# Optimization experiments

Hardware: AMD Instinct MI355X
Metric: run time of the kernel (lower is better)

## Reference

```python
import jax, jax.numpy as jnp
import numpy as np

D_MODEL = 1024
NUM_HEADS = 16
HEAD_DIM = D_MODEL // NUM_HEADS


def setup_inputs() -> dict:
    key = jax.random.key(0)
    k1, k2, k3 = jax.random.split(key, 3)
    B, T = 4, 2048
    x = jax.random.normal(k1, (B, T, D_MODEL), dtype=jnp.float32)
    # nn.Linear weights: out = x @ W.T; store torch-layout [out_features, in_features]
    w_qkv = jax.random.normal(k2, (3 * D_MODEL, D_MODEL), dtype=jnp.float32) * (D_MODEL ** -0.5)
    w_proj = jax.random.normal(k3, (D_MODEL, D_MODEL), dtype=jnp.float32) * (D_MODEL ** -0.5)
    return {"x": x, "w_qkv": w_qkv, "w_proj": w_proj}


def reference(x, w_qkv, w_proj):
    B, T, C = x.shape
    H, Dh = NUM_HEADS, HEAD_DIM
    qkv = jnp.einsum('btc,fc->btf', x, w_qkv)          # [B,T,3C]
    q, k, v = jnp.split(qkv, 3, axis=2)
    # [B,T,C] -> [B,H,T,Dh]
    q = q.reshape(B, T, H, Dh).transpose(0, 2, 1, 3)
    k = k.reshape(B, T, H, Dh).transpose(0, 2, 1, 3)
    v = v.reshape(B, T, H, Dh).transpose(0, 2, 1, 3)
    scale = Dh ** -0.5
    att = jnp.einsum('bhqd,bhkd->bhqk', q, k) * scale  # [B,H,T,T]
    causal = jnp.tril(jnp.ones((T, T), dtype=bool))
    att = jnp.where(causal, att, -jnp.inf)
    att = jax.nn.softmax(att, axis=-1)
    y = jnp.einsum('bhqk,bhkd->bhqd', att, v)          # [B,H,T,Dh]
    y = y.transpose(0, 2, 1, 3).reshape(B, T, C)
    return jnp.einsum('btc,oc->bto', y, w_proj)
```

## Files before the change

### kernel.cpp

```cpp
#include <hip/hip_runtime.h>
#include <stdint.h>
#include <math.h>

typedef __bf16 bf16;
typedef __bf16 bf16x4 __attribute__((ext_vector_type(4)));
typedef __bf16 bf16x8 __attribute__((ext_vector_type(8)));
typedef float f32x4 __attribute__((ext_vector_type(4)));

#define MFMA16(a, b, c) __builtin_amdgcn_mfma_f32_16x16x32_bf16((a), (b), (c), 0, 0, 0)

typedef __attribute__((address_space(1))) void* as1v;
typedef __attribute__((address_space(3))) void* as3v;

__device__ __forceinline__ void async_ld16(const void* g, void* l) {
  __builtin_amdgcn_global_load_lds((as1v)(uintptr_t)g,
                                   (as3v)(unsigned int)(uintptr_t)l, 16, 0, 0);
}

__global__ __launch_bounds__(256) void cast3_k(const float* __restrict__ x,
                                               const float* __restrict__ wq,
                                               const float* __restrict__ wp,
                                               bf16* __restrict__ xb,
                                               bf16* __restrict__ wqb,
                                               bf16* __restrict__ wpb) {
  const long i = (long)blockIdx.x * 256 + threadIdx.x;
  const float4* src;
  bf16x4* dst;
  long off;
  if (i < 2097152L) {
    src = (const float4*)x;  dst = (bf16x4*)xb;  off = i;
  } else if (i < 2097152L + 786432L) {
    src = (const float4*)wq; dst = (bf16x4*)wqb; off = i - 2097152L;
  } else {
    src = (const float4*)wp; dst = (bf16x4*)wpb; off = i - 2097152L - 786432L;
  }
  float4 v = src[off];
  bf16x4 o;
  o[0] = (bf16)v.x; o[1] = (bf16)v.y; o[2] = (bf16)v.z; o[3] = (bf16)v.w;
  dst[off] = o;
}

__global__ __launch_bounds__(256) void gemm_qkv(const bf16* __restrict__ A,
                                                const bf16* __restrict__ Bm,
                                                bf16* __restrict__ qb,
                                                bf16* __restrict__ kb,
                                                bf16* __restrict__ vth) {
  __shared__ bf16 As[128 * 32];
  __shared__ bf16 Bs[128 * 32];
  const int tid  = threadIdx.x;
  const int lane = tid & 63;
  const int wv   = tid >> 6;
  const int lr   = lane & 15;
  const int quad = lane >> 4;
  const int wm   = (wv >> 1) * 64;
  const int wn   = (wv & 1) * 64;
  const long m0 = (long)blockIdx.y * 128;
  const long n0 = (long)blockIdx.x * 128;

  const f32x4 fzero = {0.f, 0.f, 0.f, 0.f};
  f32x4 acc[4][4];
#pragma unroll
  for (int i = 0; i < 4; ++i)
#pragma unroll
    for (int j = 0; j < 4; ++j) acc[i][j] = fzero;

  const int r0 = wv * 32 + (lane >> 2);
  const int c0 = (lane & 3) * 8;

  for (int k0 = 0; k0 < 1024; k0 += 32) {
    __syncthreads();
    async_ld16(&A[(m0 + r0) * 1024 + k0 + c0],        &As[wv * 1024]);
    async_ld16(&A[(m0 + r0 + 16) * 1024 + k0 + c0],   &As[wv * 1024 + 512]);
    async_ld16(&Bm[(n0 + r0) * 1024 + k0 + c0],       &Bs[wv * 1024]);
    async_ld16(&Bm[(n0 + r0 + 16) * 1024 + k0 + c0],  &Bs[wv * 1024 + 512]);
    __syncthreads();

    bf16x8 af[4], bfr[4];
#pragma unroll
    for (int mi = 0; mi < 4; ++mi)
      af[mi] = *(const bf16x8*)&As[(wm + mi * 16 + lr) * 32 + quad * 8];
#pragma unroll
    for (int ni = 0; ni < 4; ++ni)
      bfr[ni] = *(const bf16x8*)&Bs[(wn + ni * 16 + lr) * 32 + quad * 8];
#pragma unroll
    for (int mi = 0; mi < 4; ++mi)
#pragma unroll
      for (int ni = 0; ni < 4; ++ni)
        acc[mi][ni] = MFMA16(af[mi], bfr[ni], acc[mi][ni]);
  }

  const int bx = blockIdx.x;
  if (bx < 8) {
    const float kS = 0.18033688f;
#pragma unroll
    for (int mi = 0; mi < 4; ++mi) {
      const long row = m0 + wm + mi * 16 + quad * 4;
#pragma unroll
      for (int ni = 0; ni < 4; ++ni) {
        const long col = n0 + wn + ni * 16 + lr;
#pragma unroll
        for (int r = 0; r < 4; ++r) qb[(row + r) * 1024 + col] = (bf16)(acc[mi][ni][r] * kS);
      }
    }
  } else if (bx < 16) {
#pragma unroll
    for (int mi = 0; mi < 4; ++mi) {
      const long row = m0 + wm + mi * 16 + quad * 4;
#pragma unroll
      for (int ni = 0; ni < 4; ++ni) {
        const long col = n0 + wn + ni * 16 + lr - 1024;
#pragma unroll
        for (int r = 0; r < 4; ++r) kb[(row + r) * 1024 + col] = (bf16)(acc[mi][ni][r]);
      }
    }
  } else {
#pragma unroll
    for (int mi = 0; mi < 4; ++mi) {
      const long row = m0 + wm + mi * 16 + quad * 4;
      const long b = row >> 11;
      const long t = row & 2047;
#pragma unroll
      for (int ni = 0; ni < 4; ++ni) {
        const long vcol = n0 + wn + ni * 16 + lr - 2048;
        const long h = vcol >> 6, d = vcol & 63;
        bf16x4 pk;
#pragma unroll
        for (int r = 0; r < 4; ++r) pk[r] = (bf16)(acc[mi][ni][r]);
        *(bf16x4*)&vth[(((b << 4) + h) * 64 + d) * 2048 + t] = pk;
      }
    }
  }
}

template <typename OutT>
__global__ __launch_bounds__(128) void gemm_bt64(const bf16* __restrict__ A,
                                                 const bf16* __restrict__ Bm,
                                                 OutT* __restrict__ C,
                                                 int M, int N, int K) {
  __shared__ bf16 As[64 * 32];
  __shared__ bf16 Bs[128 * 32];
  const int tid  = threadIdx.x;
  const int lane = tid & 63;
  const int wv   = tid >> 6;
  const int lr   = lane & 15;
  const int quad = lane >> 4;
  const long m0 = (long)blockIdx.y * 64;
  const long n0 = (long)blockIdx.x * 128;

  const f32x4 fzero = {0.f, 0.f, 0.f, 0.f};
  f32x4 acc[4][4];
#pragma unroll
  for (int i = 0; i < 4; ++i)
#pragma unroll
    for (int j = 0; j < 4; ++j) acc[i][j] = fzero;

  const int sr = lane >> 2;
  const int sc = (lane & 3) * 8;

  for (int k0 = 0; k0 < K; k0 += 32) {
    __syncthreads();
#pragma unroll
    for (int i = 0; i < 2; ++i) {
      const int r = wv * 32 + i * 16 + sr;
      async_ld16(&A[(m0 + r) * K + k0 + sc], &As[(wv * 32 + i * 16) * 32]);
    }
#pragma unroll
    for (int j = 0; j < 4; ++j) {
      const int r = wv * 64 + j * 16 + sr;
      async_ld16(&Bm[(n0 + r) * K + k0 + sc], &Bs[(wv * 64 + j * 16) * 32]);
    }
    __syncthreads();

    bf16x8 af[4], bfr[4];
#pragma unroll
    for (int mi = 0; mi < 4; ++mi)
      af[mi] = *(const bf16x8*)&As[(mi * 16 + lr) * 32 + quad * 8];
#pragma unroll
    for (int ni = 0; ni < 4; ++ni)
      bfr[ni] = *(const bf16x8*)&Bs[(wv * 64 + ni * 16 + lr) * 32 + quad * 8];
#pragma unroll
    for (int mi = 0; mi < 4; ++mi)
#pragma unroll
      for (int ni = 0; ni < 4; ++ni)
        acc[mi][ni] = MFMA16(af[mi], bfr[ni], acc[mi][ni]);
  }

#pragma unroll
  for (int mi = 0; mi < 4; ++mi) {
    const long row = m0 + mi * 16 + quad * 4;
#pragma unroll
    for (int ni = 0; ni < 4; ++ni) {
      const long col = n0 + wv * 64 + ni * 16 + lr;
#pragma unroll
      for (int r = 0; r < 4; ++r) C[(row + r) * N + col] = (OutT)acc[mi][ni][r];
    }
  }
}

__global__ __launch_bounds__(256, 2) void flash_attn5(const bf16* __restrict__ q,
                                                      const bf16* __restrict__ k,
                                                      const bf16* __restrict__ vth,
                                                      bf16* __restrict__ y) {
  __shared__ bf16 Ks[2][64 * 64];
  __shared__ bf16 Vt[64 * 64];
  __shared__ bf16 Ps[4][32 * 72];
  const int tid  = threadIdx.x;
  const int lane = tid & 63;
  const int wv   = tid >> 6;
  const int lr   = lane & 15;
  const int quad = lane >> 4;
  const int p  = blockIdx.x;
  const int bh = blockIdx.y;
  const int b = bh >> 4, h = bh & 15;
  const bf16* qp = q + ((size_t)b * 2048) * 1024 + h * 64;
  const bf16* kp = k + ((size_t)b * 2048) * 1024 + h * 64;
  const bf16* vp = vth + (size_t)bh * 64 * 2048;
  bf16* yp = y + ((size_t)b * 2048) * 1024 + h * 64;

  const int stg_row = lane >> 3;
  const int stg_cg  = (lane & 7) ^ stg_row;
  const int swz     = lr & 7;

  bf16x8 ones;
#pragma unroll
  for (int j = 0; j < 8; ++j) ones[j] = (bf16)1.0f;
  const f32x4 fz = {0.f, 0.f, 0.f, 0.f};

  for (int half = 0; half < 2; ++half) {
    const int qt = half ? p : 15 - p;
    const int q0 = qt * 128;
    const int kb_max = 2 * qt + 1;
    const int kmax_w = 2 * qt + (wv >> 1);

    bf16x8 qf[2][2];
#pragma unroll
    for (int nq = 0; nq < 2; ++nq) {
      const int qrow = q0 + wv * 32 + nq * 16 + lr;
#pragma unroll
      for (int ds = 0; ds < 2; ++ds)
        qf[nq][ds] = *(const bf16x8*)(qp + (size_t)qrow * 1024 + ds * 32 + quad * 8);
    }

    f32x4 o[2][4];
    f32x4 lacc[2];
#pragma unroll
    for (int nq = 0; nq < 2; ++nq) {
      lacc[nq] = fz;
#pragma unroll
      for (int nf = 0; nf < 4; ++nf) o[nq][nf] = fz;
    }

    __syncthreads();
#pragma unroll
    for (int i = 0; i < 2; ++i) {
      const int r = i * 32 + wv * 8 + stg_row;
      async_ld16(kp + (size_t)r * 1024 + stg_cg * 8, &Ks[0][(i * 32 + wv * 8) * 64]);
    }

    for (int kt = 0; kt <= kb_max; ++kt) {
      const int k0 = kt * 64;
      const int cb = kt & 1;
      __syncthreads();
      if (kt < kb_max) {
#pragma unroll
        for (int i = 0; i < 2; ++i) {
          const int r = i * 32 + wv * 8 + stg_row;
          async_ld16(kp + (size_t)(k0 + 64 + r) * 1024 + stg_cg * 8,
                     &Ks[cb ^ 1][(i * 32 + wv * 8) * 64]);
        }
      }
#pragma unroll
      for (int i = 0; i < 2; ++i) {
        const int r = i * 32 + wv * 8 + stg_row;
        async_ld16(vp + (size_t)r * 2048 + k0 + stg_cg * 8, &Vt[(i * 32 + wv * 8) * 64]);
      }

      const bool act = (kt <= kmax_w);
      bf16x8 ap[2][2];
      if (act) {
        f32x4 s[2][4];
#pragma unroll
        for (int nq = 0; nq < 2; ++nq)
#pragma unroll
          for (int mi = 0; mi < 4; ++mi) s[nq][mi] = fz;
#pragma unroll
        for (int ds = 0; ds < 2; ++ds)
#pragma unroll
          for (int mi = 0; mi < 4; ++mi) {
            const bf16x8 ak =
                *(const bf16x8*)&Ks[cb][(mi * 16 + lr) * 64 + (((ds << 2) + quad) ^ swz) * 8];
            s[0][mi] = MFMA16(ak, qf[0][ds], s[0][mi]);
            s[1][mi] = MFMA16(ak, qf[1][ds], s[1][mi]);
          }

        if (kt < kmax_w) {
#pragma unroll
          for (int nq = 0; nq < 2; ++nq) {
            const int qloc = nq * 16 + lr;
#pragma unroll
            for (int mi = 0; mi < 4; ++mi) {
              bf16x4 pb;
#pragma unroll
              for (int r = 0; r < 4; ++r) pb[r] = (bf16)__builtin_amdgcn_exp2f(s[nq][mi][r]);
              *(bf16x4*)&Ps[wv][qloc * 72 + mi * 16 + quad * 4] = pb;
            }
          }
        } else {
          const int kofs = k0 - q0 - wv * 32;
#pragma unroll
          for (int nq = 0; nq < 2; ++nq) {
            const int qloc = nq * 16 + lr;
#pragma unroll
            for (int mi = 0; mi < 4; ++mi) {
              bf16x4 pb;
#pragma unroll
              for (int r = 0; r < 4; ++r) {
                float pv = __builtin_amdgcn_exp2f(s[nq][mi][r]);
                if (mi * 16 + quad * 4 + r + kofs > qloc) pv = 0.0f;
                pb[r] = (bf16)pv;
              }
              *(bf16x4*)&Ps[wv][qloc * 72 + mi * 16 + quad * 4] = pb;
            }
          }
        }
#pragma unroll
        for (int ks = 0; ks < 2; ++ks) {
          ap[0][ks] = *(const bf16x8*)&Ps[wv][(lr) * 72 + ks * 32 + quad * 8];
          ap[1][ks] = *(const bf16x8*)&Ps[wv][(16 + lr) * 72 + ks * 32 + quad * 8];
        }
      }

      __syncthreads();

      if (act) {
#pragma unroll
        for (int ks = 0; ks < 2; ++ks) {
          lacc[0] = MFMA16(ap[0][ks], ones, lacc[0]);
          lacc[1] = MFMA16(ap[1][ks], ones, lacc[1]);
#pragma unroll
          for (int nf = 0; nf < 4; ++nf) {
            const bf16x8 bv =
                *(const bf16x8*)&Vt[(nf * 16 + lr) * 64 + (((ks << 2) + quad) ^ swz) * 8];
            o[0][nf] = MFMA16(ap[0][ks], bv, o[0][nf]);
            o[1][nf] = MFMA16(ap[1][ks], bv, o[1][nf]);
          }
        }
      }
    }

#pragma unroll
    for (int nq = 0; nq < 2; ++nq)
#pragma unroll
      for (int r = 0; r < 4; ++r) {
        const float inv = __builtin_amdgcn_rcpf(lacc[nq][r]);
        const int t = q0 + wv * 32 + nq * 16 + quad * 4 + r;
#pragma unroll
        for (int nf = 0; nf < 4; ++nf)
          yp[(size_t)t * 1024 + nf * 16 + lr] = (bf16)(o[nq][nf][r] * inv);
      }
  }
}

extern "C" void kernel_launch(void* const* d_in, const int* in_sizes, int n_in,
                              void* d_out, int out_size, void* d_ws, size_t ws_size,
                              hipStream_t stream) {
  const float* x      = (const float*)d_in[0];
  const float* w_qkv  = (const float*)d_in[1];
  const float* w_proj = (const float*)d_in[2];
  float* out = (float*)d_out;
  char* ws = (char*)d_ws;

  bf16* xb   = (bf16*)(ws);
  bf16* wqkb = (bf16*)(ws + (16ull << 20));
  bf16* wpb  = (bf16*)(ws + (22ull << 20));
  bf16* qb   = (bf16*)(ws + (24ull << 20));
  bf16* kbuf = (bf16*)(ws + (40ull << 20));
  bf16* vth  = (bf16*)(ws + (56ull << 20));
  bf16* yb   = (bf16*)(ws + (72ull << 20));

  cast3_k<<<dim3(12288), 256, 0, stream>>>(x, w_qkv, w_proj, xb, wqkb, wpb);
  gemm_qkv<<<dim3(24, 64), 256, 0, stream>>>(xb, wqkb, qb, kbuf, vth);
  flash_attn5<<<dim3(8, 64), 256, 0, stream>>>(qb, kbuf, vth, yb);
  gemm_bt64<float><<<dim3(8, 128), 128, 0, stream>>>(yb, wpb, out, 8192, 1024, 1024);
}
```

Baseline: 246.8 us.

## Enlarge GEMM tiles, deepen K step, and swizzle LDS layout for QKV and proj

Both GEMMs move to larger output tiles per block: QKV goes to 256x128 and the projection to 128x128, with each wave computing 64x128. The K step grows from 32 to 64, and the LDS tiles use an XOR swizzle on 16-byte column groups to avoid bank conflicts. This raises the ratio of MFMA work to LDS and global traffic and halves the number of barriers per K. In exchange there are more accumulator registers per thread and fewer blocks in flight, so occupancy and tail effects may suffer.

```diff
diff --git a/kernel.cpp b/kernel.cpp
--- a/kernel.cpp
+++ b/kernel.cpp
@@ -40,53 +40,62 @@
   dst[off] = o;
 }
 
-__global__ __launch_bounds__(256) void gemm_qkv(const bf16* __restrict__ A,
-                                                const bf16* __restrict__ Bm,
-                                                bf16* __restrict__ qb,
-                                                bf16* __restrict__ kb,
-                                                bf16* __restrict__ vth) {
-  __shared__ bf16 As[128 * 32];
-  __shared__ bf16 Bs[128 * 32];
+__global__ __launch_bounds__(256, 2) void gemm_qkv(const bf16* __restrict__ A,
+                                                   const bf16* __restrict__ Bm,
+                                                   bf16* __restrict__ qb,
+                                                   bf16* __restrict__ kb,
+                                                   bf16* __restrict__ vth) {
+  __shared__ bf16 As[256 * 64];
+  __shared__ bf16 Bs[128 * 64];
   const int tid  = threadIdx.x;
   const int lane = tid & 63;
   const int wv   = tid >> 6;
   const int lr   = lane & 15;
   const int quad = lane >> 4;
-  const int wm   = (wv >> 1) * 64;
-  const int wn   = (wv & 1) * 64;
-  const long m0 = (long)blockIdx.y * 128;
+  const long m0 = (long)blockIdx.y * 256;
   const long n0 = (long)blockIdx.x * 128;
 
-  const f32x4 fzero = {0.f, 0.f, 0.f, 0.f};
-  f32x4 acc[4][4];
+  const int srow = lane >> 3;
+  const int scg  = (lane & 7) ^ srow;
+  const int swz  = lr & 7;
+
+  const f32x4 fz = {0.f, 0.f, 0.f, 0.f};
+  f32x4 acc[4][8];
 #pragma unroll
   for (int i = 0; i < 4; ++i)
 #pragma unroll
-    for (int j = 0; j < 4; ++j) acc[i][j] = fzero;
-
-  const int r0 = wv * 32 + (lane >> 2);
-  const int c0 = (lane & 3) * 8;
-
-  for (int k0 = 0; k0 < 1024; k0 += 32) {
-    __syncthreads();
-    async_ld16(&A[(m0 + r0) * 1024 + k0 + c0],        &As[wv * 1024]);
-    async_ld16(&A[(m0 + r0 + 16) * 1024 + k0 + c0],   &As[wv * 1024 + 512]);
-    async_ld16(&Bm[(n0 + r0) * 1024 + k0 + c0],       &Bs[wv * 1024]);
-    async_ld16(&Bm[(n0 + r0 + 16) * 1024 + k0 + c0],  &Bs[wv * 1024 + 512]);
-    __syncthreads();
-
-    bf16x8 af[4], bfr[4];
-#pragma unroll
-    for (int mi = 0; mi < 4; ++mi)
-      af[mi] = *(const bf16x8*)&As[(wm + mi * 16 + lr) * 32 + quad * 8];
-#pragma unroll
-    for (int ni = 0; ni < 4; ++ni)
-      bfr[ni] = *(const bf16x8*)&Bs[(wn + ni * 16 + lr) * 32 + quad * 8];
-#pragma unroll
-    for (int mi = 0; mi < 4; ++mi)
-#pragma unroll
-      for (int ni = 0; ni < 4; ++ni)
-        acc[mi][ni] = MFMA16(af[mi], bfr[ni], acc[mi][ni]);
+    for (int j = 0; j < 8; ++j) acc[i][j] = fz;
+
+  for (int k0 = 0; k0 < 1024; k0 += 64) {
+    __syncthreads();
+#pragma unroll
+    for (int i = 0; i < 8; ++i) {
+      const int rb = wv * 64 + i * 8;
+      async_ld16(&A[(m0 + rb + srow) * 1024 + k0 + scg * 8], &As[rb * 64]);
+    }
+#pragma unroll
+    for (int i = 0; i < 4; ++i) {
+      const int rb = wv * 32 + i * 8;
+      async_ld16(&Bm[(n0 + rb + srow) * 1024 + k0 + scg * 8], &Bs[rb * 64]);
+    }
+    __syncthreads();
+
+#pragma unroll
+    for (int ds = 0; ds < 2; ++ds) {
+      const int slot = ((ds << 2) + quad) ^ swz;
+      bf16x8 af[4], bfr[8];
+#pragma unroll
+      for (int mi = 0; mi < 4; ++mi)
+        af[mi] = *(const bf16x8*)&As[(wv * 64 + mi * 16 + lr) * 64 + slot * 8];
+#pragma unroll
+      for (int ni = 0; ni < 8; ++ni)
+        bfr[ni] = *(const bf16x8*)&Bs[(ni * 16 + lr) * 64 + slot * 8];
+#pragma unroll
+      for (int mi = 0; mi < 4; ++mi)
+#pragma unroll
+        for (int ni = 0; ni < 8; ++ni)
+          acc[mi][ni] = MFMA16(af[mi], bfr[ni], acc[mi][ni]);
+    }
   }
 
   const int bx = blockIdx.x;
@@ -94,10 +103,10 @@
     const float kS = 0.18033688f;
 #pragma unroll
     for (int mi = 0; mi < 4; ++mi) {
-      const long row = m0 + wm + mi * 16 + quad * 4;
-#pragma unroll
-      for (int ni = 0; ni < 4; ++ni) {
-        const long col = n0 + wn + ni * 16 + lr;
+      const long row = m0 + wv * 64 + mi * 16 + quad * 4;
+#pragma unroll
+      for (int ni = 0; ni < 8; ++ni) {
+        const long col = n0 + ni * 16 + lr;
 #pragma unroll
         for (int r = 0; r < 4; ++r) qb[(row + r) * 1024 + col] = (bf16)(acc[mi][ni][r] * kS);
       }
@@ -105,10 +114,10 @@
   } else if (bx < 16) {
 #pragma unroll
     for (int mi = 0; mi < 4; ++mi) {
-      const long row = m0 + wm + mi * 16 + quad * 4;
-#pragma unroll
-      for (int ni = 0; ni < 4; ++ni) {
-        const long col = n0 + wn + ni * 16 + lr - 1024;
+      const long row = m0 + wv * 64 + mi * 16 + quad * 4;
+#pragma unroll
+      for (int ni = 0; ni < 8; ++ni) {
+        const long col = n0 + ni * 16 + lr - 1024;
 #pragma unroll
         for (int r = 0; r < 4; ++r) kb[(row + r) * 1024 + col] = (bf16)(acc[mi][ni][r]);
       }
@@ -116,12 +125,12 @@
   } else {
 #pragma unroll
     for (int mi = 0; mi < 4; ++mi) {
-      const long row = m0 + wm + mi * 16 + quad * 4;
+      const long row = m0 + wv * 64 + mi * 16 + quad * 4;
       const long b = row >> 11;
       const long t = row & 2047;
 #pragma unroll
-      for (int ni = 0; ni < 4; ++ni) {
-        const long vcol = n0 + wn + ni * 16 + lr - 2048;
+      for (int ni = 0; ni < 8; ++ni) {
+        const long vcol = n0 + ni * 16 + lr - 2048;
         const long h = vcol >> 6, d = vcol & 63;
         bf16x4 pk;
 #pragma unroll
@@ -132,67 +141,66 @@
   }
 }
 
-template <typename OutT>
-__global__ __launch_bounds__(128) void gemm_bt64(const bf16* __restrict__ A,
-                                                 const bf16* __restrict__ Bm,
-                                                 OutT* __restrict__ C,
-                                                 int M, int N, int K) {
-  __shared__ bf16 As[64 * 32];
-  __shared__ bf16 Bs[128 * 32];
+__global__ __launch_bounds__(128, 2) void gemm_proj(const bf16* __restrict__ A,
+                                                    const bf16* __restrict__ Bm,
+                                                    float* __restrict__ C) {
+  __shared__ bf16 As[128 * 64];
+  __shared__ bf16 Bs[128 * 64];
   const int tid  = threadIdx.x;
   const int lane = tid & 63;
   const int wv   = tid >> 6;
   const int lr   = lane & 15;
   const int quad = lane >> 4;
-  const long m0 = (long)blockIdx.y * 64;
+  const long m0 = (long)blockIdx.y * 128;
   const long n0 = (long)blockIdx.x * 128;
 
-  const f32x4 fzero = {0.f, 0.f, 0.f, 0.f};
-  f32x4 acc[4][4];
+  const int srow = lane >> 3;
+  const int scg  = (lane & 7) ^ srow;
+  const int swz  = lr & 7;
+
+  const f32x4 fz = {0.f, 0.f, 0.f, 0.f};
+  f32x4 acc[4][8];
 #pragma unroll
   for (int i = 0; i < 4; ++i)
 #pragma unroll
-    for (int j = 0; j < 4; ++j) acc[i][j] = fzero;
-
-  const int sr = lane >> 2;
-  const int sc = (lane & 3) * 8;
-
-  for (int k0 = 0; k0 < K; k0 += 32) {
-    __syncthreads();
-#pragma unroll
-    for (int i = 0; i < 2; ++i) {
-      const int r = wv * 32 + i * 16 + sr;
-      async_ld16(&A[(m0 + r) * K + k0 + sc], &As[(wv * 32 + i * 16) * 32]);
-    }
-#pragma unroll
-    for (int j = 0; j < 4; ++j) {
-      const int r = wv * 64 + j * 16 + sr;
-      async_ld16(&Bm[(n0 + r) * K + k0 + sc], &Bs[(wv * 64 + j * 16) * 32]);
-    }
-    __syncthreads();
-
-    bf16x8 af[4], bfr[4];
-#pragma unroll
-    for (int mi = 0; mi < 4; ++mi)
-      af[mi] = *(const bf16x8*)&As[(mi * 16 + lr) * 32 + quad * 8];
-#pragma unroll
-    for (int ni = 0; ni < 4; ++ni)
-      bfr[ni] = *(const bf16x8*)&Bs[(wv * 64 + ni * 16 + lr) * 32 + quad * 8];
-#pragma unroll
-    for (int mi = 0; mi < 4; ++mi)
-#pragma unroll
-      for (int ni = 0; ni < 4; ++ni)
-        acc[mi][ni] = MFMA16(af[mi], bfr[ni], acc[mi][ni]);
+    for (int j = 0; j < 8; ++j) acc[i][j] = fz;
+
+  for (int k0 = 0; k0 < 1024; k0 += 64) {
+    __syncthreads();
+#pragma unroll
+    for (int i = 0; i < 8; ++i) {
+      const int rb = wv * 64 + i * 8;
+      async_ld16(&A[(m0 + rb + srow) * 1024 + k0 + scg * 8], &As[rb * 64]);
+      async_ld16(&Bm[(n0 + rb + srow) * 1024 + k0 + scg * 8], &Bs[rb * 64]);
+    }
+    __syncthreads();
+
+#pragma unroll
+    for (int ds = 0; ds < 2; ++ds) {
+      const int slot = ((ds << 2) + quad) ^ swz;
+      bf16x8 af[4], bfr[8];
+#pragma unroll
+      for (int mi = 0; mi < 4; ++mi)
+        af[mi] = *(const bf16x8*)&As[(wv * 64 + mi * 16 + lr) * 64 + slot * 8];
+#pragma unroll
+      for (int ni = 0; ni < 8; ++ni)
+        bfr[ni] = *(const bf16x8*)&Bs[(ni * 16 + lr) * 64 + slot * 8];
+#pragma unroll
+      for (int mi = 0; mi < 4; ++mi)
+#pragma unroll
+        for (int ni = 0; ni < 8; ++ni)
+          acc[mi][ni] = MFMA16(af[mi], bfr[ni], acc[mi][ni]);
+    }
   }
 
 #pragma unroll
   for (int mi = 0; mi < 4; ++mi) {
-    const long row = m0 + mi * 16 + quad * 4;
-#pragma unroll
-    for (int ni = 0; ni < 4; ++ni) {
-      const long col = n0 + wv * 64 + ni * 16 + lr;
-#pragma unroll
-      for (int r = 0; r < 4; ++r) C[(row + r) * N + col] = (OutT)acc[mi][ni][r];
+    const long row = m0 + wv * 64 + mi * 16 + quad * 4;
+#pragma unroll
+    for (int ni = 0; ni < 8; ++ni) {
+      const long col = n0 + ni * 16 + lr;
+#pragma unroll
+      for (int r = 0; r < 4; ++r) C[(row + r) * 1024 + col] = acc[mi][ni][r];
     }
   }
 }
@@ -379,7 +387,7 @@
   bf16* yb   = (bf16*)(ws + (72ull << 20));
 
   cast3_k<<<dim3(12288), 256, 0, stream>>>(x, w_qkv, w_proj, xb, wqkb, wpb);
-  gemm_qkv<<<dim3(24, 64), 256, 0, stream>>>(xb, wqkb, qb, kbuf, vth);
+  gemm_qkv<<<dim3(24, 32), 256, 0, stream>>>(xb, wqkb, qb, kbuf, vth);
   flash_attn5<<<dim3(8, 64), 256, 0, stream>>>(qb, kbuf, vth, yb);
-  gemm_bt64<float><<<dim3(8, 128), 128, 0, stream>>>(yb, wpb, out, 8192, 1024, 1024);
-}
+  gemm_proj<<<dim3(8, 64), 128, 0, stream>>>(yb, wpb, out);
+}
```

New measurement: 234.5 us. 1.05x faster.
